# Performance work log

Hardware: AMD Instinct MI355X
Metric: run time of the kernel (lower is better)

## Reference

```python
import jax, jax.numpy as jnp
import numpy as np

INPUT_SIZE = 1024
HIDDEN = 1024


def setup_inputs() -> dict:
    key = jax.random.key(0)
    kx, kq, kk, kv, kbq, kbk, kbv = jax.random.split(key, 7)
    bound = 1.0 / np.sqrt(INPUT_SIZE)  # torch Linear default init range
    x = jax.random.normal(kx, (4, 2048, INPUT_SIZE), dtype=jnp.float32)
    Wq = jax.random.uniform(kq, (INPUT_SIZE, HIDDEN), minval=-bound, maxval=bound, dtype=jnp.float32)
    Wk = jax.random.uniform(kk, (INPUT_SIZE, HIDDEN), minval=-bound, maxval=bound, dtype=jnp.float32)
    Wv = jax.random.uniform(kv, (INPUT_SIZE, HIDDEN), minval=-bound, maxval=bound, dtype=jnp.float32)
    bq = jax.random.uniform(kbq, (HIDDEN,), minval=-bound, maxval=bound, dtype=jnp.float32)
    bk = jax.random.uniform(kbk, (HIDDEN,), minval=-bound, maxval=bound, dtype=jnp.float32)
    bv = jax.random.uniform(kbv, (HIDDEN,), minval=-bound, maxval=bound, dtype=jnp.float32)
    return {"x": x, "Wq": Wq, "bq": bq, "Wk": Wk, "bk": bk, "Wv": Wv, "bv": bv}


def reference(x, Wq, bq, Wk, bk, Wv, bv):
    # x: [b, s, d_in]; projections -> [b, s, h]
    Q = jnp.einsum("bsd,dh->bsh", x, Wq) + bq
    K = jnp.einsum("bsd,dh->bsh", x, Wk) + bk
    V = jnp.einsum("bsd,dh->bsh", x, Wv) + bv
    scale = jnp.asarray(HIDDEN, jnp.float32) ** 0.5
    scores = jnp.einsum("bqh,bkh->bqk", Q, K) / scale  # [b, s, s]
    probs = jax.nn.softmax(scores, axis=-1)
    return jnp.einsum("bqk,bkh->bqh", probs, V)  # [b, s, h]
```

## Files before the change

### kernel.cpp

```cpp
#include <hip/hip_runtime.h>
#include <hip/hip_bf16.h>
#include <stdint.h>


typedef __attribute__((ext_vector_type(8))) short bf16x8;
typedef __attribute__((ext_vector_type(4))) float f32x4;

#define BATCH 4
#define SEQ   2048
#define DIM   1024
#define MROWS (BATCH * SEQ)
#define NQKV  (3 * DIM)

#define BARR  __builtin_amdgcn_s_barrier()
#define LGKM0 asm volatile("s_waitcnt lgkmcnt(0)" ::: "memory")
#define VM6   asm volatile("s_waitcnt vmcnt(6)" ::: "memory")

__device__ __forceinline__ unsigned short f2bf(float f) {
    union { float f; uint32_t u; } v; v.f = f;
    uint32_t u = v.u;
    return (unsigned short)((u + 0x7FFFu + ((u >> 16) & 1u)) >> 16);
}
__device__ __forceinline__ float bf2f(unsigned short b) {
    union { uint32_t u; float f; } v; v.u = ((uint32_t)b) << 16;
    return v.f;
}

__device__ __forceinline__ void gload16(const unsigned short* g, unsigned short* l) {
    __builtin_amdgcn_global_load_lds(
        (const __attribute__((address_space(1))) unsigned int*)g,
        (__attribute__((address_space(3))) unsigned int*)l,
        16, 0, 0);
}

__global__ void cast_x_kernel(const float* __restrict__ x,
                              unsigned short* __restrict__ xb, int n8) {
    int i = blockIdx.x * blockDim.x + threadIdx.x;
    if (i >= n8) return;
    const float4* p = reinterpret_cast<const float4*>(x) + (size_t)i * 2;
    float4 a = p[0], b = p[1];
    union { unsigned short u[8]; uint4 v; } o;
    o.u[0] = f2bf(a.x); o.u[1] = f2bf(a.y); o.u[2] = f2bf(a.z); o.u[3] = f2bf(a.w);
    o.u[4] = f2bf(b.x); o.u[5] = f2bf(b.y); o.u[6] = f2bf(b.z); o.u[7] = f2bf(b.w);
    reinterpret_cast<uint4*>(xb)[i] = o.v;
}

__global__ void transpose_w_kernel(const float* __restrict__ Wq,
                                   const float* __restrict__ Wk,
                                   const float* __restrict__ Wv,
                                   unsigned short* __restrict__ Wt) {
    __shared__ float tile[32][33];
    const float* W = (blockIdx.z == 0) ? Wq : (blockIdx.z == 1 ? Wk : Wv);
    int d0 = blockIdx.x * 32, h0 = blockIdx.y * 32;
    int t = threadIdx.x;
    int lr = t >> 5, lc = t & 31;
    #pragma unroll
    for (int r = 0; r < 4; ++r) {
        int row = r * 8 + lr;
        tile[row][lc] = W[(size_t)(d0 + row) * DIM + h0 + lc];
    }
    __syncthreads();
    unsigned short* out = Wt + (size_t)blockIdx.z * DIM * DIM;
    #pragma unroll
    for (int r = 0; r < 4; ++r) {
        int hrow = r * 8 + lr;
        out[(size_t)(h0 + hrow) * DIM + d0 + lc] = f2bf(tile[lc][hrow]);
    }
}

__global__ void concat_bias_kernel(const float* __restrict__ bq,
                                   const float* __restrict__ bk,
                                   const float* __restrict__ bv,
                                   float* __restrict__ out) {
    int i = blockIdx.x * blockDim.x + threadIdx.x;
    if (i >= NQKV) return;
    out[i] = (i < DIM) ? bq[i] : (i < 2 * DIM ? bk[i - DIM] : bv[i - 2 * DIM]);
}

template <bool OUT_BF16, bool HAS_BIAS, bool BATCH_B>
__global__ __launch_bounds__(512, 2) void gemm128n_kernel(
    const unsigned short* __restrict__ A, int lda,
    const unsigned short* __restrict__ B, int ldb, size_t bStride,
    void* __restrict__ Cv, int ldc,
    const float* __restrict__ bias, float scale, int K)
{
    __shared__ unsigned short lds[49152];

    const int gx   = gridDim.x;
    const int nwg  = gx * gridDim.y;
    const int flat = blockIdx.y * gx + blockIdx.x;
    const int cpx  = nwg >> 3;
    const int swz  = (flat & 7) * cpx + (flat >> 3);
    const int m0   = (swz / gx) * 256;
    const int n0   = (swz % gx) * 128;

    if (BATCH_B) B += (size_t)(m0 >> 11) * bStride;

    const int t = threadIdx.x, l = t & 63, w = t >> 6;
    const int wr = w >> 1, wc = w & 1;

    const int srow = w * 16 + (l >> 3);
    const int scol = ((l & 7) ^ ((l >> 3) & 7)) << 3;
    const unsigned short* gA = A + (size_t)(m0 + srow) * lda + scol;
    const unsigned short* gB = B + (size_t)(n0 + srow) * ldb + scol;

    auto STG_A = [&](int hf, int bufb, int tj) {
        const unsigned short* g = gA + (size_t)hf * 128 * lda + (size_t)tj * 64;
        unsigned short* d = &lds[bufb + hf * 8192 + w * 1024];
        gload16(g, d);
        gload16(g + (size_t)8 * lda, d + 512);
    };
    auto STG_B = [&](int bufb, int tj) {
        const unsigned short* g = gB + (size_t)tj * 64;
        unsigned short* d = &lds[bufb + 16384 + w * 1024];
        gload16(g, d);
        gload16(g + (size_t)8 * ldb, d + 512);
    };

    const int r15 = l & 15;
    const int sw0 = ((l >> 4) ^ (r15 & 7)) << 3;
    const int sw1 = sw0 ^ 32;
    const int aBase = (wr >> 1) * 8192 + ((wr & 1) * 64 + r15) * 64;
    const int bBase = 16384 + (wc * 64 + r15) * 64;

    bf16x8 Ae[4][2], Ao[4][2], Be[4][2], Bo[4][2];
    f32x4  acc[4][4] = {};

    auto RDA = [&](int bufb, bf16x8 (&Af)[4][2]) {
        const unsigned short* p = &lds[bufb + aBase];
        #pragma unroll
        for (int fm = 0; fm < 4; ++fm) {
            Af[fm][0] = *reinterpret_cast<const bf16x8*>(&p[fm * 1024 + sw0]);
            Af[fm][1] = *reinterpret_cast<const bf16x8*>(&p[fm * 1024 + sw1]);
        }
    };
    auto RDB = [&](int bufb, bf16x8 (&Bf)[4][2]) {
        const unsigned short* p = &lds[bufb + bBase];
        #pragma unroll
        for (int fn = 0; fn < 4; ++fn) {
            Bf[fn][0] = *reinterpret_cast<const bf16x8*>(&p[fn * 1024 + sw0]);
            Bf[fn][1] = *reinterpret_cast<const bf16x8*>(&p[fn * 1024 + sw1]);
        }
    };
    auto MF = [&](bf16x8 (&Af)[4][2], int fh, bf16x8 (&Bf)[4][2]) {
        __builtin_amdgcn_s_setprio(1);
        #pragma unroll
        for (int fm = 2 * fh; fm < 2 * fh + 2; ++fm)
            #pragma unroll
            for (int fn = 0; fn < 4; ++fn)
                #pragma unroll
                for (int ks = 0; ks < 2; ++ks)
                    acc[fm][fn] = __builtin_amdgcn_mfma_f32_16x16x32_bf16(
                        Af[fm][ks], Bf[fn][ks], acc[fm][fn], 0, 0, 0);
        __builtin_amdgcn_s_setprio(0);
    };

    const int NT = K >> 6, NI = K >> 7;
    const int B1 = 24576;

    STG_A(0, 0, 0); STG_A(1, 0, 0); STG_B(0, 0);
    STG_A(0, B1, 1); STG_A(1, B1, 1);
    VM6;
    BARR;

    for (int i = 0; i < NI; ++i) {
        const int T  = 2 * i;
        const int t2 = (T + 2 < NT) ? T + 2 : NT - 1;
        const int t3 = (T + 3 < NT) ? T + 3 : NT - 1;
        RDA(0, Ae);
        STG_B(B1, T + 1);
        VM6; BARR; LGKM0;
        if (i) MF(Ao, 1, Bo);
        BARR;
        RDB(0, Be);
        STG_A(0, 0, t2); STG_A(1, 0, t2);
        VM6; BARR; LGKM0;
        MF(Ae, 0, Be);
        BARR;
        RDA(B1, Ao);
        STG_B(0, t2);
        VM6; BARR; LGKM0;
        MF(Ae, 1, Be);
        BARR;
        RDB(B1, Bo);
        STG_A(0, B1, t3); STG_A(1, B1, t3);
        VM6; BARR; LGKM0;
        MF(Ao, 0, Bo);
        BARR;
    }
    MF(Ao, 1, Bo);

    const int rql = (l >> 4) << 2;
    #pragma unroll
    for (int fn = 0; fn < 4; ++fn) {
        const int col = n0 + wc * 64 + fn * 16 + r15;
        const float bv = HAS_BIAS ? bias[col] : 0.0f;
        #pragma unroll
        for (int fm = 0; fm < 4; ++fm)
            #pragma unroll
            for (int r = 0; r < 4; ++r) {
                const int row = m0 + wr * 64 + fm * 16 + rql + r;
                const float v = acc[fm][fn][r] * scale + bv;
                if (OUT_BF16)
                    reinterpret_cast<unsigned short*>(Cv)[(size_t)row * ldc + col] = f2bf(v);
                else
                    reinterpret_cast<float*>(Cv)[(size_t)row * ldc + col] = v;
            }
    }
}

template <bool HAS_BIAS>
__global__ __launch_bounds__(512, 2) void gemm256p_kernel(
    const unsigned short* __restrict__ A, int lda, size_t strideA,
    const unsigned short* __restrict__ B, int ldb, size_t strideB,
    unsigned short* __restrict__ C, int ldc, size_t strideC,
    const float* __restrict__ bias, float scale, int K)
{
    __shared__ unsigned short lds[65536];

    const int gx   = gridDim.x;
    const int nwg  = gx * gridDim.y;
    const int flat = blockIdx.y * gx + blockIdx.x;
    const int cpx  = nwg >> 3;
    const int swz  = (flat & 7) * cpx + (flat >> 3);
    const int m0   = (swz / gx) * 256;
    const int n0   = (swz % gx) * 256;

    A += (size_t)blockIdx.z * strideA;
    B += (size_t)blockIdx.z * strideB;

    const int t = threadIdx.x, l = t & 63, w = t >> 6;
    const int wr = w >> 2, wc = w & 3;

    const int srow = w * 16 + (l >> 3);
    const int scol = ((l & 7) ^ ((l >> 3) & 7)) << 3;
    const unsigned short* gA = A + (size_t)(m0 + srow) * lda + scol;
    const unsigned short* gB = B + (size_t)(n0 + srow) * ldb + scol;

    auto STG = [&](int op, int hf, int bufb, int tj) {
        const int ld = op ? ldb : lda;
        const unsigned short* g = (op ? gB : gA) + (size_t)hf * 128 * ld + (size_t)tj * 64;
        unsigned short* d = &lds[bufb + op * 16384 + hf * 8192 + w * 1024];
        gload16(g, d);
        gload16(g + (size_t)8 * ld, d + 512);
    };

    const int r15 = l & 15;
    const int kq  = l >> 4;
    const int sw0 = (kq ^ (r15 & 7)) << 3;
    const int sw1 = sw0 ^ 32;
    const int rbA = (wr * 64 + r15) * 64;
    const int rbB = (wc * 32 + r15) * 64;

    bf16x8 Ar[4][2], Bl[2][2], Bh[2][2];
    f32x4  acc[2][2][4][2] = {};

    auto RDA = [&](int bufb, int q) {
        const unsigned short* p = &lds[bufb + q * 8192 + rbA];
        #pragma unroll
        for (int fm = 0; fm < 4; ++fm) {
            Ar[fm][0] = *reinterpret_cast<const bf16x8*>(&p[fm * 1024 + sw0]);
            Ar[fm][1] = *reinterpret_cast<const bf16x8*>(&p[fm * 1024 + sw1]);
        }
    };
    auto RDB = [&](int bufb, int q, bf16x8 (&Bd)[2][2]) {
        const unsigned short* p = &lds[bufb + 16384 + q * 8192 + rbB];
        #pragma unroll
        for (int fn = 0; fn < 2; ++fn) {
            Bd[fn][0] = *reinterpret_cast<const bf16x8*>(&p[fn * 1024 + sw0]);
            Bd[fn][1] = *reinterpret_cast<const bf16x8*>(&p[fn * 1024 + sw1]);
        }
    };
    auto MQ = [&](f32x4 (&ac)[4][2], bf16x8 (&Bd)[2][2]) {
        __builtin_amdgcn_s_setprio(1);
        #pragma unroll
        for (int fm = 0; fm < 4; ++fm)
            #pragma unroll
            for (int fn = 0; fn < 2; ++fn)
                #pragma unroll
                for (int ks = 0; ks < 2; ++ks)
                    ac[fm][fn] = __builtin_amdgcn_mfma_f32_16x16x32_bf16(
                        Ar[fm][ks], Bd[fn][ks], ac[fm][fn], 0, 0, 0);
        __builtin_amdgcn_s_setprio(0);
    };

    const int NT = K >> 6, NI = K >> 7;

    STG(0, 0, 0, 0); STG(1, 0, 0, 0); STG(0, 1, 0, 0); STG(1, 1, 0, 0);
    STG(0, 0, 32768, 1); STG(1, 0, 32768, 1); STG(1, 1, 32768, 1);
    VM6;
    BARR;

    for (int i = 0; i < NI; ++i) {
        const int T  = 2 * i;
        const int t2 = (T + 2 < NT) ? T + 2 : NT - 1;
        const bool more = (i + 1 < NI);
        RDA(0, 0); RDB(0, 0, Bl);
        STG(0, 1, 32768, T + 1);
        BARR; LGKM0;
        MQ(acc[0][0], Bl);
        BARR;
        RDB(0, 1, Bh);
        STG(0, 0, 0, t2);
        BARR; LGKM0;
        MQ(acc[0][1], Bh);
        BARR;
        RDA(0, 1);
        STG(1, 0, 0, t2);
        BARR; LGKM0;
        MQ(acc[1][1], Bh);
        BARR;
        STG(1, 1, 0, t2);
        VM6;
        BARR;
        MQ(acc[1][0], Bl);
        BARR;
        RDA(32768, 0); RDB(32768, 0, Bl);
        STG(0, 1, 0, t2);
        BARR; LGKM0;
        MQ(acc[0][0], Bl);
        BARR;
        RDB(32768, 1, Bh);
        if (more) STG(0, 0, 32768, T + 3);
        BARR; LGKM0;
        MQ(acc[0][1], Bh);
        BARR;
        RDA(32768, 1);
        if (more) STG(1, 0, 32768, T + 3);
        BARR; LGKM0;
        MQ(acc[1][1], Bh);
        BARR;
        if (more) STG(1, 1, 32768, T + 3);
        VM6;
        BARR;
        MQ(acc[1][0], Bl);
        BARR;
    }

    const int rql = (l >> 4) << 2;
    unsigned short* Cp = C + (size_t)blockIdx.z * strideC;
    #pragma unroll
    for (int qm = 0; qm < 2; ++qm)
        #pragma unroll
        for (int qn = 0; qn < 2; ++qn)
            #pragma unroll
            for (int fn = 0; fn < 2; ++fn) {
                const int col = n0 + qn * 128 + wc * 32 + fn * 16 + r15;
                const float bv = HAS_BIAS ? bias[col] : 0.0f;
                #pragma unroll
                for (int fm = 0; fm < 4; ++fm)
                    #pragma unroll
                    for (int r = 0; r < 4; ++r) {
                        const int row = m0 + qm * 128 + wr * 64 + fm * 16 + rql + r;
                        Cp[(size_t)row * ldc + col] =
                            f2bf(acc[qm][qn][fm][fn][r] * scale + bv);
                    }
            }
}

__global__ __launch_bounds__(256) void softmax_kernel(unsigned short* __restrict__ S) {
    __shared__ float red[8];
    unsigned short* p = S + (size_t)blockIdx.x * SEQ;
    const int t = threadIdx.x;
    union { uint4 v; unsigned short u[8]; } in;
    in.v = reinterpret_cast<const uint4*>(p)[t];
    float f[8];
    float m = -1e30f;
    #pragma unroll
    for (int i = 0; i < 8; ++i) { f[i] = bf2f(in.u[i]); m = fmaxf(m, f[i]); }
    #pragma unroll
    for (int off = 32; off > 0; off >>= 1) m = fmaxf(m, __shfl_xor(m, off));
    if ((t & 63) == 0) red[t >> 6] = m;
    __syncthreads();
    m = fmaxf(fmaxf(red[0], red[1]), fmaxf(red[2], red[3]));
    float s = 0.0f;
    #pragma unroll
    for (int i = 0; i < 8; ++i) { f[i] = __expf(f[i] - m); s += f[i]; }
    #pragma unroll
    for (int off = 32; off > 0; off >>= 1) s += __shfl_xor(s, off);
    __syncthreads();
    if ((t & 63) == 0) red[4 + (t >> 6)] = s;
    __syncthreads();
    s = (red[4] + red[5]) + (red[6] + red[7]);
    const float inv = 1.0f / s;
    union { uint4 v; unsigned short u[8]; } o;
    #pragma unroll
    for (int i = 0; i < 8; ++i) o.u[i] = f2bf(f[i] * inv);
    reinterpret_cast<uint4*>(p)[t] = o.v;
}

__global__ void transpose_v_kernel(const unsigned short* __restrict__ QKV,
                                   unsigned short* __restrict__ Vt) {
    __shared__ unsigned short tile[32][34];
    const int b = blockIdx.z;
    const int s0 = blockIdx.x * 32, h0 = blockIdx.y * 32;
    const int t = threadIdx.x, lr = t >> 5, lc = t & 31;
    const unsigned short* in = QKV + (size_t)b * SEQ * NQKV + 2 * DIM;
    #pragma unroll
    for (int r = 0; r < 4; ++r) {
        int si = r * 8 + lr;
        tile[si][lc] = in[(size_t)(s0 + si) * NQKV + h0 + lc];
    }
    __syncthreads();
    unsigned short* out = Vt + (size_t)b * DIM * SEQ;
    #pragma unroll
    for (int r = 0; r < 4; ++r) {
        int hi = r * 8 + lr;
        out[(size_t)(h0 + hi) * SEQ + s0 + lc] = tile[lc][hi];
    }
}

extern "C" void kernel_launch(void* const* d_in, const int* in_sizes, int n_in,
                              void* d_out, int out_size, void* d_ws, size_t ws_size,
                              hipStream_t stream) {
    const float* x  = (const float*)d_in[0];
    const float* Wq = (const float*)d_in[1];
    const float* bq = (const float*)d_in[2];
    const float* Wk = (const float*)d_in[3];
    const float* bk = (const float*)d_in[4];
    const float* Wv = (const float*)d_in[5];
    const float* bv = (const float*)d_in[6];
    float* out = (float*)d_out;
    char* ws = (char*)d_ws;

    const size_t OFF_XB   = 0;
    const size_t OFF_WT   = 16777216;
    const size_t OFF_BIAS = 23068672;
    const size_t OFF_QKV  = 23080960;
    const size_t OFF_S    = 73412608;

    unsigned short* xb   = (unsigned short*)(ws + OFF_XB);
    unsigned short* Wt   = (unsigned short*)(ws + OFF_WT);
    float*          bcat = (float*)(ws + OFF_BIAS);
    unsigned short* qkv  = (unsigned short*)(ws + OFF_QKV);
    unsigned short* Smat = (unsigned short*)(ws + OFF_S);
    unsigned short* Vt   = (unsigned short*)(ws + OFF_XB);

    cast_x_kernel<<<(MROWS * DIM / 8 + 255) / 256, 256, 0, stream>>>(x, xb, MROWS * DIM / 8);
    transpose_w_kernel<<<dim3(32, 32, 3), 256, 0, stream>>>(Wq, Wk, Wv, Wt);
    concat_bias_kernel<<<12, 256, 0, stream>>>(bq, bk, bv, bcat);

    gemm128n_kernel<true, true, false><<<dim3(NQKV / 128, MROWS / 256), 512, 0, stream>>>(
        xb, DIM, Wt, DIM, 0, qkv, NQKV, bcat, 1.0f, DIM);

    gemm256p_kernel<false><<<dim3(SEQ / 256, SEQ / 256, BATCH), 512, 0, stream>>>(
        qkv, NQKV, (size_t)SEQ * NQKV,
        qkv + DIM, NQKV, (size_t)SEQ * NQKV,
        Smat, SEQ, (size_t)SEQ * SEQ,
        nullptr, 1.0f / 32.0f, DIM);

    softmax_kernel<<<BATCH * SEQ, 256, 0, stream>>>(Smat);

    transpose_v_kernel<<<dim3(SEQ / 32, DIM / 32, BATCH), 256, 0, stream>>>(qkv, Vt);
    gemm128n_kernel<false, false, true><<<dim3(DIM / 128, MROWS / 256), 512, 0, stream>>>(
        Smat, SEQ, Vt, SEQ, (size_t)DIM * SEQ, out, DIM, nullptr, 1.0f, SEQ);
}
```

Measured before the change: 163.5 us.

## Fuse V transpose into V projection epilogue and split QK projection

The QKV projection is split in two. Q and K are computed with the 256-wide GEMM kernel into a packed QK buffer. V gets its own GEMM launch whose epilogue stages the tile in LDS and writes it out already transposed (Vt), so the separate transpose_v kernel and its round trip of V through global memory go away. The cost is an extra GEMM launch, LDS staging with strided reads in the epilogue, and a different tile shape for the QK projection.

```diff
diff --git a/kernel.cpp b/kernel.cpp
--- a/kernel.cpp
+++ b/kernel.cpp
@@ -77,7 +77,7 @@
     out[i] = (i < DIM) ? bq[i] : (i < 2 * DIM ? bk[i - DIM] : bv[i - 2 * DIM]);
 }
 
-template <bool OUT_BF16, bool HAS_BIAS, bool BATCH_B>
+template <bool OUT_BF16, bool HAS_BIAS, bool BATCH_B, bool V_TRANS>
 __global__ __launch_bounds__(512, 2) void gemm128n_kernel(
     const unsigned short* __restrict__ A, int lda,
     const unsigned short* __restrict__ B, int ldb, size_t bStride,
@@ -191,6 +191,36 @@
     MF(Ao, 1, Bo);
 
     const int rql = (l >> 4) << 2;
+
+    if constexpr (V_TRANS) {
+        #pragma unroll
+        for (int fn = 0; fn < 4; ++fn) {
+            const int col = wc * 64 + fn * 16 + r15;
+            const float bv = HAS_BIAS ? bias[n0 + col] : 0.0f;
+            #pragma unroll
+            for (int fm = 0; fm < 4; ++fm)
+                #pragma unroll
+                for (int r = 0; r < 4; ++r) {
+                    const int sr = wr * 64 + fm * 16 + rql + r;
+                    lds[sr * 130 + col] = f2bf(acc[fm][fn][r] * scale + bv);
+                }
+        }
+        __syncthreads();
+        const int h  = t & 127;
+        const int s0 = (t >> 7) * 64;
+        unsigned short* dst = reinterpret_cast<unsigned short*>(Cv)
+            + ((size_t)(m0 >> 11) * DIM + n0 + h) * SEQ + (m0 & 2047) + s0;
+        #pragma unroll
+        for (int j8 = 0; j8 < 8; ++j8) {
+            union { unsigned short u[8]; uint4 v; } pk;
+            #pragma unroll
+            for (int j = 0; j < 8; ++j)
+                pk.u[j] = lds[(s0 + j8 * 8 + j) * 130 + h];
+            *reinterpret_cast<uint4*>(dst + j8 * 8) = pk.v;
+        }
+        return;
+    }
+
     #pragma unroll
     for (int fn = 0; fn < 4; ++fn) {
         const int col = n0 + wc * 64 + fn * 16 + r15;
@@ -389,27 +419,6 @@
     reinterpret_cast<uint4*>(p)[t] = o.v;
 }
 
-__global__ void transpose_v_kernel(const unsigned short* __restrict__ QKV,
-                                   unsigned short* __restrict__ Vt) {
-    __shared__ unsigned short tile[32][34];
-    const int b = blockIdx.z;
-    const int s0 = blockIdx.x * 32, h0 = blockIdx.y * 32;
-    const int t = threadIdx.x, lr = t >> 5, lc = t & 31;
-    const unsigned short* in = QKV + (size_t)b * SEQ * NQKV + 2 * DIM;
-    #pragma unroll
-    for (int r = 0; r < 4; ++r) {
-        int si = r * 8 + lr;
-        tile[si][lc] = in[(size_t)(s0 + si) * NQKV + h0 + lc];
-    }
-    __syncthreads();
-    unsigned short* out = Vt + (size_t)b * DIM * SEQ;
-    #pragma unroll
-    for (int r = 0; r < 4; ++r) {
-        int hi = r * 8 + lr;
-        out[(size_t)(h0 + hi) * SEQ + s0 + lc] = tile[lc][hi];
-    }
-}
-
 extern "C" void kernel_launch(void* const* d_in, const int* in_sizes, int n_in,
                               void* d_out, int out_size, void* d_ws, size_t ws_size,
                               hipStream_t stream) {
@@ -426,32 +435,35 @@
     const size_t OFF_XB   = 0;
     const size_t OFF_WT   = 16777216;
     const size_t OFF_BIAS = 23068672;
-    const size_t OFF_QKV  = 23080960;
-    const size_t OFF_S    = 73412608;
+    const size_t OFF_QK   = 23080960;
+    const size_t OFF_S    = 56635392;
+    const size_t OFF_VT   = 90189824;
 
     unsigned short* xb   = (unsigned short*)(ws + OFF_XB);
     unsigned short* Wt   = (unsigned short*)(ws + OFF_WT);
     float*          bcat = (float*)(ws + OFF_BIAS);
-    unsigned short* qkv  = (unsigned short*)(ws + OFF_QKV);
+    unsigned short* qk   = (unsigned short*)(ws + OFF_QK);
     unsigned short* Smat = (unsigned short*)(ws + OFF_S);
-    unsigned short* Vt   = (unsigned short*)(ws + OFF_XB);
+    unsigned short* Vt   = (unsigned short*)(ws + OFF_VT);
 
     cast_x_kernel<<<(MROWS * DIM / 8 + 255) / 256, 256, 0, stream>>>(x, xb, MROWS * DIM / 8);
     transpose_w_kernel<<<dim3(32, 32, 3), 256, 0, stream>>>(Wq, Wk, Wv, Wt);
     concat_bias_kernel<<<12, 256, 0, stream>>>(bq, bk, bv, bcat);
 
-    gemm128n_kernel<true, true, false><<<dim3(NQKV / 128, MROWS / 256), 512, 0, stream>>>(
-        xb, DIM, Wt, DIM, 0, qkv, NQKV, bcat, 1.0f, DIM);
+    gemm256p_kernel<true><<<dim3(2048 / 256, MROWS / 256, 1), 512, 0, stream>>>(
+        xb, DIM, 0, Wt, DIM, 0, qk, 2048, 0, bcat, 1.0f, DIM);
+
+    gemm128n_kernel<true, true, false, true><<<dim3(DIM / 128, MROWS / 256), 512, 0, stream>>>(
+        xb, DIM, Wt + (size_t)2048 * DIM, DIM, 0, Vt, SEQ, bcat + 2048, 1.0f, DIM);
 
     gemm256p_kernel<false><<<dim3(SEQ / 256, SEQ / 256, BATCH), 512, 0, stream>>>(
-        qkv, NQKV, (size_t)SEQ * NQKV,
-        qkv + DIM, NQKV, (size_t)SEQ * NQKV,
+        qk, 2048, (size_t)SEQ * 2048,
+        qk + 1024, 2048, (size_t)SEQ * 2048,
         Smat, SEQ, (size_t)SEQ * SEQ,
         nullptr, 1.0f / 32.0f, DIM);
 
     softmax_kernel<<<BATCH * SEQ, 256, 0, stream>>>(Smat);
 
-    transpose_v_kernel<<<dim3(SEQ / 32, DIM / 32, BATCH), 256, 0, stream>>>(qkv, Vt);
-    gemm128n_kernel<false, false, true><<<dim3(DIM / 128, MROWS / 256), 512, 0, stream>>>(
+    gemm128n_kernel<false, false, true, false><<<dim3(DIM / 128, MROWS / 256), 512, 0, stream>>>(
         Smat, SEQ, Vt, SEQ, (size_t)DIM * SEQ, out, DIM, nullptr, 1.0f, SEQ);
 }
```

New measurement: 159.5 us. 1.02x faster.
